# Kernel optimization log

Hardware: AMD Instinct MI355X
Metric: run time of the kernel (lower is better)

Reference implementation:

```python
import jax, jax.numpy as jnp
import numpy as np

C = 64      # in_channels
NX = 432    # pseudo-image x dim
NY = 496    # pseudo-image y dim
B = 4       # batch size
M_PER = 12000  # pillars per sample (KITTI PointPillars max)


def setup_inputs() -> dict:
    key = jax.random.key(0)
    rng = np.random.default_rng(0)
    feats = jax.random.normal(key, (B * M_PER, C), dtype=jnp.float32)
    # Build per-sample UNIQUE spatial indices (real voxelization never emits
    # duplicate pillar coords within a sample; duplicates would make the
    # scatter-set nondeterministic).
    coords = []
    for b in range(B):
        flat = rng.permutation(NX * NY)[:M_PER]
        x = flat // NY
        y = flat % NY
        z = np.zeros_like(x)
        coords.append(np.stack([z, y, x], axis=1))  # (M_PER, 3) in z,y,x order
    batch_indices = jnp.asarray(np.concatenate(coords, axis=0), dtype=jnp.int32)
    sample_indices = jnp.asarray(np.repeat(np.arange(B), M_PER), dtype=jnp.int32)
    return {
        "batch_pillar_features": feats,
        "batch_indices": batch_indices,
        "sample_indices": sample_indices,
        "batch_size": B,
    }


def reference(batch_pillar_features, batch_indices, sample_indices, batch_size):
    # Single fused scatter over the whole batch: flatten (sample, x, y) into
    # one linear index into a (B*NX*NY, C) canvas, then reshape.
    spatial = batch_indices[:, 2].astype(jnp.int32) * NY + batch_indices[:, 1].astype(jnp.int32)
    flat = sample_indices.astype(jnp.int32) * (NX * NY) + spatial  # (M,)
    canvas = jnp.zeros((batch_size * NX * NY, C), dtype=batch_pillar_features.dtype)
    canvas = canvas.at[flat].set(batch_pillar_features)            # scatter rows
    canvas = canvas.reshape(batch_size, NX, NY, C).transpose(0, 3, 1, 2)  # (B,C,NX,NY)
    return jnp.flip(canvas, axis=2)  # torch.flip(dims=[2])
```

## Files before the change

kernel.cpp:

```cpp
#include <hip/hip_runtime.h>

#define C_CH 64
#define NX 432
#define NY 496
#define NYQ 124
#define PLANEQ (NX * NYQ)
#define SLOTS 64
#define NXCD 8


__global__ void scatter_idx_kernel(const int* __restrict__ bidx,
                                   const int* __restrict__ sidx,
                                   int* __restrict__ map, int M) {
    int m = blockIdx.x * blockDim.x + threadIdx.x;
    if (m >= M) return;
    int y = bidx[3 * m + 1];
    int x = bidx[3 * m + 2];
    int s = sidx[m];
    map[(size_t)s * (NX * NY) + (size_t)(NX - 1 - x) * NY + y] = m;
}

__global__ __launch_bounds__(256) void column_write_kernel(
        const float* __restrict__ feats,
        const int* __restrict__ map,
        float4* __restrict__ out, int nwg) {
    __shared__ int4  map4[NYQ];
    __shared__ int   slot_m[SLOTS];
    __shared__ float rows[SLOTS + 1][C_CH + 1];
    __shared__ int   cnt, ovf;

    int* map_row = (int*)map4;
    const int chunk = nwg / NXCD;
    const int blk = (blockIdx.x % NXCD) * chunk + blockIdx.x / NXCD;
    const int b   = blk / NX;
    const int xo  = blk - b * NX;
    const int tid = threadIdx.x;

    if (tid == 0) { cnt = 0; ovf = 0; }
    if (tid < C_CH) rows[SLOTS][tid] = 0.0f;
    __syncthreads();

    const int* mp = map + ((size_t)b * NX + xo) * NY;
    for (int y = tid; y < NY; y += 256) {
        int m = mp[y];
        int v = SLOTS;
        if (m >= 0) {
            int s = atomicAdd(&cnt, 1);
            if (s < SLOTS) { slot_m[s] = m; v = s; }
            else { v = -2 - m; ovf = 1; }
        }
        map_row[y] = v;
    }
    __syncthreads();

    const int n = (cnt < SLOTS) ? cnt : SLOTS;
    for (int e = tid; e < n * C_CH; e += 256) {
        int s = e >> 6;
        int c = e & (C_CH - 1);
        rows[s][c] = feats[(size_t)slot_m[s] * C_CH + c];
    }
    __syncthreads();

    const int t    = tid & 127;
    const int cof  = tid >> 7;
    int4 mm = make_int4(SLOTS, SLOTS, SLOTS, SLOTS);
    if (t < NYQ) mm = map4[t];
    float4* ob = out + ((size_t)b * C_CH * NX + xo) * NYQ + t;

    if (!ovf) {
        #pragma unroll 8
        for (int c2 = 0; c2 < C_CH / 2; ++c2) {
            int c = (c2 << 1) + cof;
            if (t < NYQ) {
                float4 v;
                v.x = rows[mm.x][c];
                v.y = rows[mm.y][c];
                v.z = rows[mm.z][c];
                v.w = rows[mm.w][c];
                ob[(size_t)c * PLANEQ] = v;
            }
        }
    } else {
        for (int c2 = 0; c2 < C_CH / 2; ++c2) {
            int c = (c2 << 1) + cof;
            if (t < NYQ) {
                float4 v;
                v.x = (mm.x >= 0) ? rows[mm.x][c] : feats[(size_t)(-2 - mm.x) * C_CH + c];
                v.y = (mm.y >= 0) ? rows[mm.y][c] : feats[(size_t)(-2 - mm.y) * C_CH + c];
                v.z = (mm.z >= 0) ? rows[mm.z][c] : feats[(size_t)(-2 - mm.z) * C_CH + c];
                v.w = (mm.w >= 0) ? rows[mm.w][c] : feats[(size_t)(-2 - mm.w) * C_CH + c];
                ob[(size_t)c * PLANEQ] = v;
            }
        }
    }
}


__global__ void zero_out_kernel(float4* __restrict__ out, int nq) {
    int i = blockIdx.x * blockDim.x + threadIdx.x;
    if (i < nq) out[i] = make_float4(0.f, 0.f, 0.f, 0.f);
}

__global__ void scatter_feats_kernel(const float* __restrict__ feats,
                                     const int* __restrict__ bidx,
                                     const int* __restrict__ sidx,
                                     float* __restrict__ out, int M) {
    int tid = blockIdx.x * blockDim.x + threadIdx.x;
    if (tid >= M * C_CH) return;
    int m = tid >> 6;
    int c = tid & (C_CH - 1);
    int y = bidx[3 * m + 1];
    int x = bidx[3 * m + 2];
    int s = sidx[m];
    size_t o = (((size_t)s * C_CH + c) * NX + (NX - 1 - x)) * NY + y;
    out[o] = feats[tid];
}

extern "C" void kernel_launch(void* const* d_in, const int* in_sizes, int n_in,
                              void* d_out, int out_size, void* d_ws, size_t ws_size,
                              hipStream_t stream) {
    const float* feats = (const float*)d_in[0];
    const int*   bidx  = (const int*)d_in[1];
    const int*   sidx  = (const int*)d_in[2];
    float*       out   = (float*)d_out;

    const int M = in_sizes[0] / C_CH;
    const int B = out_size / (C_CH * NX * NY);

    const size_t map_elems = (size_t)B * NX * NY;
    const size_t map_bytes = map_elems * sizeof(int);
    const int nwg = B * NX;

    if (ws_size >= map_bytes && (nwg % NXCD) == 0) {
        int* map = (int*)d_ws;
        hipMemsetAsync(map, 0xFF, map_bytes, stream);
        scatter_idx_kernel<<<(M + 255) / 256, 256, 0, stream>>>(bidx, sidx, map, M);
        column_write_kernel<<<nwg, 256, 0, stream>>>(
            feats, map, (float4*)out, nwg);
    } else {
        int nq = out_size / 4;
        zero_out_kernel<<<(nq + 255) / 256, 256, 0, stream>>>((float4*)out, nq);
        int nt = M * C_CH;
        scatter_feats_kernel<<<(nt + 255) / 256, 256, 0, stream>>>(
            feats, bidx, sidx, out, M);
    }
}
```

Baseline: 45.08 us.

## Replace dense index map with per-column compact pillar lists

Instead of memsetting and scattering into a dense B*NX*NY int map, the index kernel appends packed (pillar, y) entries into per-column lists with atomic counters. The column kernel then reads only its column's count and list rather than scanning all NY map entries. This removes the large memset and the dense map read, in exchange for global atomics and a fixed per-column list capacity. It also drops the XCD-aware block remapping, and it assumes equal pillars per sample (mper = M/B) and that no column overflows the list capacity.

```diff
diff --git a/kernel.cpp b/kernel.cpp
--- a/kernel.cpp
+++ b/kernel.cpp
@@ -6,50 +6,52 @@
 #define NYQ 124
 #define PLANEQ (NX * NYQ)
 #define SLOTS 64
-#define NXCD 8
+#define CAP 512
 
 
 __global__ void scatter_idx_kernel(const int* __restrict__ bidx,
                                    const int* __restrict__ sidx,
-                                   int* __restrict__ map, int M) {
+                                   int* __restrict__ colcnt,
+                                   int* __restrict__ colist,
+                                   int M, int mper) {
     int m = blockIdx.x * blockDim.x + threadIdx.x;
     if (m >= M) return;
     int y = bidx[3 * m + 1];
     int x = bidx[3 * m + 2];
     int s = sidx[m];
-    map[(size_t)s * (NX * NY) + (size_t)(NX - 1 - x) * NY + y] = m;
+    int j = m - s * mper;
+    int col = s * NX + (NX - 1 - x);
+    int slot = atomicAdd(&colcnt[col], 1);
+    if (slot < CAP) colist[col * CAP + slot] = (j << 9) | y;
 }
 
 __global__ __launch_bounds__(256) void column_write_kernel(
         const float* __restrict__ feats,
-        const int* __restrict__ map,
-        float4* __restrict__ out, int nwg) {
+        const int* __restrict__ colcnt,
+        const int* __restrict__ colist,
+        float4* __restrict__ out, int mper) {
     __shared__ int4  map4[NYQ];
     __shared__ int   slot_m[SLOTS];
     __shared__ float rows[SLOTS + 1][C_CH + 1];
-    __shared__ int   cnt, ovf;
+    int* map_row = (int*)map4;
 
-    int* map_row = (int*)map4;
-    const int chunk = nwg / NXCD;
-    const int blk = (blockIdx.x % NXCD) * chunk + blockIdx.x / NXCD;
-    const int b   = blk / NX;
-    const int xo  = blk - b * NX;
+    const int col = blockIdx.x;
+    const int b   = col / NX;
+    const int xo  = col - b * NX;
     const int tid = threadIdx.x;
+    const int mbase = b * mper;
 
-    if (tid == 0) { cnt = 0; ovf = 0; }
+    const int cnt = colcnt[col];
+    for (int i = tid; i < NY; i += 256) map_row[i] = SLOTS;
     if (tid < C_CH) rows[SLOTS][tid] = 0.0f;
     __syncthreads();
-
-    const int* mp = map + ((size_t)b * NX + xo) * NY;
-    for (int y = tid; y < NY; y += 256) {
-        int m = mp[y];
-        int v = SLOTS;
-        if (m >= 0) {
-            int s = atomicAdd(&cnt, 1);
-            if (s < SLOTS) { slot_m[s] = m; v = s; }
-            else { v = -2 - m; ovf = 1; }
-        }
-        map_row[y] = v;
+    const int* cl = colist + (size_t)col * CAP;
+    for (int e = tid; e < cnt; e += 256) {
+        int v = cl[e];
+        int y = v & 511;
+        int j = v >> 9;
+        if (e < SLOTS) { slot_m[e] = mbase + j; map_row[y] = e; }
+        else map_row[y] = -2 - j;
     }
     __syncthreads();
 
@@ -61,13 +63,13 @@
     }
     __syncthreads();
 
-    const int t    = tid & 127;
-    const int cof  = tid >> 7;
+    const int t   = tid & 127;
+    const int cof = tid >> 7;
     int4 mm = make_int4(SLOTS, SLOTS, SLOTS, SLOTS);
     if (t < NYQ) mm = map4[t];
     float4* ob = out + ((size_t)b * C_CH * NX + xo) * NYQ + t;
 
-    if (!ovf) {
+    if (cnt <= SLOTS) {
         #pragma unroll 8
         for (int c2 = 0; c2 < C_CH / 2; ++c2) {
             int c = (c2 << 1) + cof;
@@ -85,10 +87,10 @@
             int c = (c2 << 1) + cof;
             if (t < NYQ) {
                 float4 v;
-                v.x = (mm.x >= 0) ? rows[mm.x][c] : feats[(size_t)(-2 - mm.x) * C_CH + c];
-                v.y = (mm.y >= 0) ? rows[mm.y][c] : feats[(size_t)(-2 - mm.y) * C_CH + c];
-                v.z = (mm.z >= 0) ? rows[mm.z][c] : feats[(size_t)(-2 - mm.z) * C_CH + c];
-                v.w = (mm.w >= 0) ? rows[mm.w][c] : feats[(size_t)(-2 - mm.w) * C_CH + c];
+                v.x = (mm.x >= 0) ? rows[mm.x][c] : feats[(size_t)(mbase + (-2 - mm.x)) * C_CH + c];
+                v.y = (mm.y >= 0) ? rows[mm.y][c] : feats[(size_t)(mbase + (-2 - mm.y)) * C_CH + c];
+                v.z = (mm.z >= 0) ? rows[mm.z][c] : feats[(size_t)(mbase + (-2 - mm.z)) * C_CH + c];
+                v.w = (mm.w >= 0) ? rows[mm.w][c] : feats[(size_t)(mbase + (-2 - mm.w)) * C_CH + c];
                 ob[(size_t)c * PLANEQ] = v;
             }
         }
@@ -126,17 +128,20 @@
 
     const int M = in_sizes[0] / C_CH;
     const int B = out_size / (C_CH * NX * NY);
+    const int mper = M / B;
+    const int ncol = B * NX;
 
-    const size_t map_elems = (size_t)B * NX * NY;
-    const size_t map_bytes = map_elems * sizeof(int);
-    const int nwg = B * NX;
+    const size_t cnt_bytes = (size_t)ncol * sizeof(int);
+    const size_t ws_need   = cnt_bytes + (size_t)ncol * CAP * sizeof(int);
 
-    if (ws_size >= map_bytes && (nwg % NXCD) == 0) {
-        int* map = (int*)d_ws;
-        hipMemsetAsync(map, 0xFF, map_bytes, stream);
-        scatter_idx_kernel<<<(M + 255) / 256, 256, 0, stream>>>(bidx, sidx, map, M);
-        column_write_kernel<<<nwg, 256, 0, stream>>>(
-            feats, map, (float4*)out, nwg);
+    if (ws_size >= ws_need && mper < (1 << 14)) {
+        int* colcnt = (int*)d_ws;
+        int* colist = colcnt + ncol;
+        hipMemsetAsync(colcnt, 0, cnt_bytes, stream);
+        scatter_idx_kernel<<<(M + 255) / 256, 256, 0, stream>>>(
+            bidx, sidx, colcnt, colist, M, mper);
+        column_write_kernel<<<ncol, 256, 0, stream>>>(
+            feats, colcnt, colist, (float4*)out, mper);
     } else {
         int nq = out_size / 4;
         zero_out_kernel<<<(nq + 255) / 256, 256, 0, stream>>>((float4*)out, nq);
```

After: 48.14 us. 6.8% more time.
